# Performance work log

Hardware: AMD Instinct MI355X
Metric: run time of the kernel (lower is better)

The kernel has to match this reference:

```python
import jax, jax.numpy as jnp
import numpy as np

E, NH, NL, NP, DFFN = 256, 8, 4, 4, 1024
HD = E // NH
EPS = 1e-5
SHAPES = np.array([[128, 128], [64, 64], [32, 32], [16, 16]], np.int32)


def layer_norm(x, w, b):
    m = x.mean(-1, keepdims=True)
    v = ((x - m) ** 2).mean(-1, keepdims=True)
    return (x - m) * jax.lax.rsqrt(v + EPS) * w + b


def mha(q, k, v, in_w, in_b, out_w, out_b):
    # q: [Lq, B, E], k/v: [Lk, B, E]  (torch nn.MultiheadAttention, seq-first)
    Lq, B, _ = q.shape
    wq, wk, wv = jnp.split(in_w, 3, axis=0)
    bq, bk, bv = jnp.split(in_b, 3)
    qh = (q @ wq.T + bq).reshape(Lq, B, NH, HD)
    kh = (k @ wk.T + bk).reshape(k.shape[0], B, NH, HD)
    vh = (v @ wv.T + bv).reshape(v.shape[0], B, NH, HD)
    scores = jnp.einsum('qbhd,kbhd->bhqk', qh, kh) / jnp.sqrt(jnp.asarray(HD, q.dtype))
    attn = jax.nn.softmax(scores, axis=-1)
    out = jnp.einsum('bhqk,kbhd->qbhd', attn, vh).reshape(Lq, B, E)
    return out @ out_w.T + out_b


def deform_core(value, spatial_shapes, loc, w):
    # value: [bs, Lv, NH, HD]; loc: [bs, nq, NH, NL, NP, 2] in [0,1]; w: [bs, nq, NH, NL, NP]
    bs, _, nh, hd = value.shape
    nq = loc.shape[1]
    out = jnp.zeros((bs, nq, nh, hd), value.dtype)
    start = 0
    for l in range(len(spatial_shapes)):
        H, W = int(spatial_shapes[l][0]), int(spatial_shapes[l][1])
        val = value[:, start:start + H * W]  # [bs, H*W, nh, hd]
        start += H * W
        # grid_sample align_corners=False convention: pixel = loc*size - 0.5
        x = loc[:, :, :, l, :, 0] * W - 0.5  # [bs, nq, nh, NP]
        y = loc[:, :, :, l, :, 1] * H - 0.5
        x0 = jnp.floor(x); y0 = jnp.floor(y)
        lx = x - x0; ly = y - y0
        x0i = x0.astype(jnp.int32); y0i = y0.astype(jnp.int32)

        def gather(yi, xi):
            valid = ((xi >= 0) & (xi < W) & (yi >= 0) & (yi < H)).astype(value.dtype)
            idx = jnp.clip(yi, 0, H - 1) * W + jnp.clip(xi, 0, W - 1)  # [bs, nq, nh, NP]
            idx2 = idx.transpose(0, 1, 3, 2).reshape(bs, nq * NP, nh)
            g = jnp.take_along_axis(val, idx2[..., None], axis=1)  # [bs, nq*NP, nh, hd]
            g = g.reshape(bs, nq, NP, nh, hd).transpose(0, 1, 3, 2, 4)  # [bs, nq, nh, NP, hd]
            return g * valid[..., None]

        samp = (gather(y0i, x0i) * ((1 - lx) * (1 - ly))[..., None]
                + gather(y0i, x0i + 1) * (lx * (1 - ly))[..., None]
                + gather(y0i + 1, x0i) * ((1 - lx) * ly)[..., None]
                + gather(y0i + 1, x0i + 1) * (lx * ly)[..., None])
        out = out + (samp * w[:, :, :, l, :, None]).sum(axis=3)
    return out.reshape(bs, nq, nh * hd)


def fwd(tgt, tgt_pos, ref_pts, memory_support, memory,
        sa_in_w, sa_in_b, sa_out_w, sa_out_b,
        cs_in_w, cs_in_b, cs_out_w, cs_out_b,
        so_w, so_b, aw_w, aw_b, vp_w, vp_b, op_w, op_b,
        norm1_w, norm1_b, norm2_w, norm2_b, csn_w, csn_b, norm3_w, norm3_b,
        lin1_w, lin1_b, lin2_w, lin2_b, spatial_shapes):
    # --- self attention ---
    q = tgt + tgt_pos
    tgt = layer_norm(tgt + mha(q, q, tgt, sa_in_w, sa_in_b, sa_out_w, sa_out_b), norm2_w, norm2_b)
    # --- cross attention on support tokens ---
    ms = memory_support.transpose(1, 0, 2)  # [Ls, bs, E]
    tgt = layer_norm(tgt + mha(tgt + tgt_pos, ms, ms, cs_in_w, cs_in_b, cs_out_w, cs_out_b), csn_w, csn_b)
    # --- multi-scale deformable cross attention ---
    query = (tgt + tgt_pos).transpose(1, 0, 2)  # [bs, nq, E]
    ref = ref_pts.transpose(1, 0, 2, 3)  # [bs, nq, NL, 4]
    bs, nq = query.shape[:2]
    val = (memory.transpose(1, 0, 2) @ vp_w.T + vp_b).reshape(bs, -1, NH, HD)
    off = (query @ so_w.T + so_b).reshape(bs, nq, NH, NL, NP, 2)
    aw = jax.nn.softmax((query @ aw_w.T + aw_b).reshape(bs, nq, NH, NL * NP), axis=-1)
    aw = aw.reshape(bs, nq, NH, NL, NP)
    loc = ref[:, :, None, :, None, :2] + off / NP * ref[:, :, None, :, None, 2:] * 0.5
    out = deform_core(val, spatial_shapes, loc, aw) @ op_w.T + op_b  # [bs, nq, E]
    tgt = layer_norm(tgt + out.transpose(1, 0, 2), norm1_w, norm1_b)
    # --- FFN ---
    h = jax.nn.relu(tgt @ lin1_w.T + lin1_b)
    return layer_norm(tgt + (h @ lin2_w.T + lin2_b), norm3_w, norm3_b)


def setup_inputs():
    nq, bs, Ls = 900, 8, 100
    Lv = int((SHAPES[:, 0] * SHAPES[:, 1]).sum())
    keys = iter(jax.random.split(jax.random.key(0), 64))
    f = lambda *s: jax.random.normal(next(keys), s, jnp.float32)
    w = lambda o, i: f(o, i) * 0.02
    # sampling-offset bias mirrors torch _reset_parameters grid init
    thetas = np.arange(NH, dtype=np.float32) * (2.0 * np.pi / NH)
    grid = np.stack([np.cos(thetas), np.sin(thetas)], -1)
    grid = grid / np.abs(grid).max(-1, keepdims=True)
    grid = np.tile(grid.reshape(NH, 1, 1, 2), (1, NL, NP, 1)) * np.arange(1, NP + 1, dtype=np.float32).reshape(1, 1, NP, 1)
    xy = jax.random.uniform(next(keys), (nq, bs, NL, 2))
    wh = jax.random.uniform(next(keys), (nq, bs, NL, 2)) * 0.2 + 0.02
    return dict(
        tgt=f(nq, bs, E) * 0.1,
        tgt_pos=f(nq, bs, E) * 0.1,
        tgt_reference_points=jnp.concatenate([xy, wh], -1),
        memory_support=f(bs, Ls, E) * 0.1,
        memory=f(Lv, bs, E) * 0.1,
        memory_spatial_shapes=SHAPES,
        sa_in_w=w(3 * E, E), sa_in_b=jnp.zeros(3 * E), sa_out_w=w(E, E), sa_out_b=jnp.zeros(E),
        cs_in_w=w(3 * E, E), cs_in_b=jnp.zeros(3 * E), cs_out_w=w(E, E), cs_out_b=jnp.zeros(E),
        so_w=f(NH * NL * NP * 2, E) * 0.01, so_b=jnp.asarray(grid.reshape(-1)),
        aw_w=f(NH * NL * NP, E) * 0.01, aw_b=jnp.zeros(NH * NL * NP),
        vp_w=w(E, E), vp_b=jnp.zeros(E), op_w=w(E, E), op_b=jnp.zeros(E),
        norm1_w=jnp.ones(E), norm1_b=jnp.zeros(E),
        norm2_w=jnp.ones(E), norm2_b=jnp.zeros(E),
        csn_w=jnp.ones(E), csn_b=jnp.zeros(E),
        norm3_w=jnp.ones(E), norm3_b=jnp.zeros(E),
        lin1_w=w(DFFN, E), lin1_b=jnp.zeros(DFFN),
        lin2_w=w(E, DFFN), lin2_b=jnp.zeros(E),
    )


def reference(tgt, tgt_pos, tgt_reference_points, memory_support, memory, memory_spatial_shapes,
              sa_in_w, sa_in_b, sa_out_w, sa_out_b, cs_in_w, cs_in_b, cs_out_w, cs_out_b,
              so_w, so_b, aw_w, aw_b, vp_w, vp_b, op_w, op_b,
              norm1_w, norm1_b, norm2_w, norm2_b, csn_w, csn_b, norm3_w, norm3_b,
              lin1_w, lin1_b, lin2_w, lin2_b):
    return fwd(tgt, tgt_pos, tgt_reference_points, memory_support, memory,
               sa_in_w, sa_in_b, sa_out_w, sa_out_b,
               cs_in_w, cs_in_b, cs_out_w, cs_out_b,
               so_w, so_b, aw_w, aw_b, vp_w, vp_b, op_w, op_b,
               norm1_w, norm1_b, norm2_w, norm2_b, csn_w, csn_b, norm3_w, norm3_b,
               lin1_w, lin1_b, lin2_w, lin2_b, SHAPES)
```

## Files before the change

### kernel.cpp

```cpp
#include <hip/hip_runtime.h>
#include <hip/hip_bf16.h>


typedef __hip_bfloat16 bf16;
typedef __attribute__((ext_vector_type(8))) short short8;
typedef __attribute__((ext_vector_type(4))) float f32x4;

__device__ __forceinline__ float toF(bf16 x) { return __bfloat162float(x); }

__device__ __forceinline__ float ldF(const void* p, size_t i, int f32mode) {
    if (f32mode) return ((const float*)p)[i];
    return __bfloat162float(((const bf16*)p)[i]);
}
__device__ __forceinline__ void stF(void* p, size_t i, int f32mode, float v) {
    if (f32mode) ((float*)p)[i] = v;
    else ((bf16*)p)[i] = __float2bfloat16(v);
}
__device__ __forceinline__ int decode(int code, int fl) { return code == 2 ? fl : code; }

__device__ __forceinline__ short f2b(float x) {
    bf16 h = __float2bfloat16(x);
    return *(short*)&h;
}

__device__ __forceinline__ short8 loadFrag8(const void* p, size_t idx, int f32m) {
    short8 r;
    if (f32m) {
        const float4* q = (const float4*)((const float*)p + idx);
        float4 u = q[0];
        float4 v = q[1];
        r[0] = f2b(u.x); r[1] = f2b(u.y); r[2] = f2b(u.z); r[3] = f2b(u.w);
        r[4] = f2b(v.x); r[5] = f2b(v.y); r[6] = f2b(v.z); r[7] = f2b(v.w);
    } else {
        r = *(const short8*)((const bf16*)p + idx);
    }
    return r;
}

__global__ __launch_bounds__(256) void detect_kernel(
    const unsigned short* __restrict__ t, int* __restrict__ flag)
{
    __shared__ int bad;
    if (threadIdx.x == 0) bad = 0;
    __syncthreads();
    int my = 0;
    for (int k = 0; k < 8; k++) {
        unsigned u = t[threadIdx.x + 256 * k];
        unsigned e = (u >> 7) & 0xFF;
        if (e >= 0xC0) my = 1;
    }
    if (my) atomicOr(&bad, 1);
    __syncthreads();
    if (threadIdx.x == 0) *flag = bad;
}

__global__ __launch_bounds__(256) void dbg_kernel(bf16* out, int n, float v)
{
    int i = blockIdx.x * 256 + threadIdx.x;
    if (i < n) out[i] = __float2bfloat16(v);
}

template <bool RELU>
__global__ __launch_bounds__(256) void mgemm_kernel(
    const void* __restrict__ A, int lda, size_t aOff, int aCode,
    const void* __restrict__ W, size_t wOff,
    const void* __restrict__ bias, size_t bOff,
    bf16* __restrict__ C, int ldc,
    int M, int N, int K, const int* __restrict__ flagp)
{
    const int fl = *flagp;
    const int am = decode(aCode, fl);
    const int tid = threadIdx.x;
    const int lane = tid & 63;
    const int wv = tid >> 6;
    const int l15 = lane & 15;
    const int quad = lane >> 4;
    const int bm = blockIdx.y * 64 + wv * 16;
    const int bn = blockIdx.x * 64;

    const int ar = min(bm + l15, M - 1);
    const size_t aBase = aOff + (size_t)ar * lda + quad * 8;

    f32x4 acc[4] = {};

    for (int k0 = 0; k0 < K; k0 += 32) {
        short8 af = loadFrag8(A, aBase + k0, am);
#pragma unroll
        for (int nt = 0; nt < 4; nt++) {
            int n = bn + nt * 16 + l15;
            short8 bfr = loadFrag8(W, wOff + (size_t)n * K + quad * 8 + k0, fl);
            acc[nt] = __builtin_amdgcn_mfma_f32_16x16x32_bf16(af, bfr, acc[nt], 0, 0, 0);
        }
    }

#pragma unroll
    for (int nt = 0; nt < 4; nt++) {
        int n = bn + nt * 16 + l15;
        float bv = ldF(bias, bOff + n, fl);
#pragma unroll
        for (int r = 0; r < 4; r++) {
            int row = bm + quad * 4 + r;
            if (row < M) {
                float v = acc[nt][r] + bv;
                if (RELU) v = fmaxf(v, 0.f);
                C[(size_t)row * ldc + n] = __float2bfloat16(v);
            }
        }
    }
}

template <bool RELU>
__global__ __launch_bounds__(512) void mgemm_lds_kernel(
    const void* __restrict__ A, int lda, size_t aOff, int aCode,
    const void* __restrict__ W, size_t wOff,
    const void* __restrict__ bias, size_t bOff,
    bf16* __restrict__ C, int ldc,
    int M, int K, const int* __restrict__ flagp)
{
    const int fl = *flagp;
    const int am = decode(aCode, fl);
    const int tid = threadIdx.x;
    const int lane = tid & 63;
    const int w = tid >> 6;
    const int l15 = lane & 15;
    const int quad = lane >> 4;
    const int wr = w >> 2;
    const int wc = w & 3;
    const int bm = blockIdx.y * 128;
    const int bn = blockIdx.x * 256;

    __shared__ short Al[128][40];
    __shared__ short Bl[256][40];

    const int sRow = tid >> 2;
    const int sCb  = (tid & 3) * 8;
    const int gArow = min(bm + sRow, M - 1);
    const size_t aRowBase = aOff + (size_t)gArow * lda + sCb;
    const size_t wRowBase0 = wOff + (size_t)(bn + sRow) * K + sCb;
    const size_t wRowBase1 = wOff + (size_t)(bn + 128 + sRow) * K + sCb;

    f32x4 acc[4][4] = {};

    for (int k0 = 0; k0 < K; k0 += 32) {
        __syncthreads();
        *(short8*)&Al[sRow][sCb]       = loadFrag8(A, aRowBase + k0, am);
        *(short8*)&Bl[sRow][sCb]       = loadFrag8(W, wRowBase0 + k0, fl);
        *(short8*)&Bl[128 + sRow][sCb] = loadFrag8(W, wRowBase1 + k0, fl);
        __syncthreads();

        short8 a0 = *(const short8*)&Al[wr * 64 +  0 + l15][quad * 8];
        short8 a1 = *(const short8*)&Al[wr * 64 + 16 + l15][quad * 8];
        short8 a2 = *(const short8*)&Al[wr * 64 + 32 + l15][quad * 8];
        short8 a3 = *(const short8*)&Al[wr * 64 + 48 + l15][quad * 8];
#pragma unroll
        for (int nt = 0; nt < 4; nt++) {
            short8 b = *(const short8*)&Bl[wc * 64 + nt * 16 + l15][quad * 8];
            acc[0][nt] = __builtin_amdgcn_mfma_f32_16x16x32_bf16(a0, b, acc[0][nt], 0, 0, 0);
            acc[1][nt] = __builtin_amdgcn_mfma_f32_16x16x32_bf16(a1, b, acc[1][nt], 0, 0, 0);
            acc[2][nt] = __builtin_amdgcn_mfma_f32_16x16x32_bf16(a2, b, acc[2][nt], 0, 0, 0);
            acc[3][nt] = __builtin_amdgcn_mfma_f32_16x16x32_bf16(a3, b, acc[3][nt], 0, 0, 0);
        }
    }

#pragma unroll
    for (int nt = 0; nt < 4; nt++) {
        int n = bn + wc * 64 + nt * 16 + l15;
        float bv = ldF(bias, bOff + n, fl);
#pragma unroll
        for (int mt = 0; mt < 4; mt++) {
#pragma unroll
            for (int r = 0; r < 4; r++) {
                int row = bm + wr * 64 + mt * 16 + quad * 4 + r;
                if (row < M) {
                    float v = acc[mt][nt][r] + bv;
                    if (RELU) v = fmaxf(v, 0.f);
                    C[(size_t)row * ldc + n] = __float2bfloat16(v);
                }
            }
        }
    }
}

__global__ __launch_bounds__(256) void add_kernel(
    const void* __restrict__ A, int aCode, const void* __restrict__ B,
    bf16* __restrict__ out, int n, const int* __restrict__ flagp)
{
    const int fl = *flagp;
    const int am = decode(aCode, fl);
    int i = blockIdx.x * 256 + threadIdx.x;
    if (i < n) out[i] = __float2bfloat16(ldF(A, i, am) + ldF(B, i, fl));
}

__global__ __launch_bounds__(256) void ln_res_kernel(
    const bf16* __restrict__ A, const void* __restrict__ R, int rCode,
    const void* __restrict__ w, const void* __restrict__ b,
    void* __restrict__ out, int oCode, const int* __restrict__ flagp)
{
    const int fl = *flagp;
    const int rm = decode(rCode, fl);
    const int om = decode(oCode, fl);
    const int r = blockIdx.x, tid = threadIdx.x;
    const size_t o = (size_t)r * 256 + tid;
    float x = toF(A[o]) + ldF(R, o, rm);
    __shared__ float red[256];
    red[tid] = x;
    __syncthreads();
    for (int st = 128; st > 0; st >>= 1) {
        if (tid < st) red[tid] += red[tid + st];
        __syncthreads();
    }
    float mean = red[0] * (1.f / 256.f);
    __syncthreads();
    float dx = x - mean;
    red[tid] = dx * dx;
    __syncthreads();
    for (int st = 128; st > 0; st >>= 1) {
        if (tid < st) red[tid] += red[tid + st];
        __syncthreads();
    }
    float var = red[0] * (1.f / 256.f);
    float y = dx * rsqrtf(var + 1e-5f) * ldF(w, tid, fl) + ldF(b, tid, fl);
    stF(out, o, om, y);
}

__global__ __launch_bounds__(256) void transpose_v_kernel(
    const bf16* __restrict__ V, int vs0, int vs1,
    bf16* __restrict__ VT, int Lk, int lkp)
{
    int i = blockIdx.x * 256 + threadIdx.x;
    int kp = i % lkp;
    int ch = i / lkp;
    int b = ch >> 8, hd = ch & 255;
    bf16 v = __float2bfloat16(0.f);
    if (kp < Lk) v = V[(size_t)kp * vs0 + (size_t)b * vs1 + hd];
    VT[i] = v;
}

__global__ __launch_bounds__(256) void fattn_kernel(
    const bf16* __restrict__ Q, int qs0, int qs1,
    const bf16* __restrict__ K, int ks0, int ks1,
    const bf16* __restrict__ VT, int lkp,
    bf16* __restrict__ O, int Lk, float scale)
{
    const int bh = blockIdx.x;
    const int b = bh >> 3, h = bh & 7;
    const int qt = blockIdx.y;
    const int tid = threadIdx.x;
    const int w = tid >> 6;
    const int lane = tid & 63;
    const int l15 = lane & 15;
    const int quad = lane >> 4;

    __shared__ short Pl[4][16][72];

    const int q0 = qt * 64 + w * 16;
    const int qr = min(q0 + l15, 899);
    short8 aq = *(const short8*)(Q + (size_t)qr * qs0 + (size_t)b * qs1 + h * 32 + quad * 8);

    f32x4 accO0 = {}, accO1 = {};
    float mrow[4] = {-1e30f, -1e30f, -1e30f, -1e30f};
    float lrow[4] = {0.f, 0.f, 0.f, 0.f};

    const bf16* Kb = K + (size_t)b * ks1 + h * 32 + quad * 8;
    const bf16* VTb = VT + (size_t)(b * 256 + h * 32) * lkp;

    const int nkt = (Lk + 63) >> 6;
    for (int kt = 0; kt < nkt; kt++) {
        const int k0 = kt * 64;
        float sv[4][4];
#pragma unroll
        for (int nt = 0; nt < 4; nt++) {
            int kk = k0 + nt * 16 + l15;
            int krow = min(kk, Lk - 1);
            short8 bk = *(const short8*)(Kb + (size_t)krow * ks0);
            f32x4 z = {};
            f32x4 s = __builtin_amdgcn_mfma_f32_16x16x32_bf16(aq, bk, z, 0, 0, 0);
            bool ok = kk < Lk;
#pragma unroll
            for (int r = 0; r < 4; r++) sv[nt][r] = ok ? s[r] * scale : -1e30f;
        }
        float mnew[4], fr[4];
#pragma unroll
        for (int r = 0; r < 4; r++) {
            float t = fmaxf(fmaxf(sv[0][r], sv[1][r]), fmaxf(sv[2][r], sv[3][r]));
            t = fmaxf(t, __shfl_xor(t, 1));
            t = fmaxf(t, __shfl_xor(t, 2));
            t = fmaxf(t, __shfl_xor(t, 4));
            t = fmaxf(t, __shfl_xor(t, 8));
            mnew[r] = fmaxf(mrow[r], t);
            fr[r] = __expf(mrow[r] - mnew[r]);
            mrow[r] = mnew[r];
        }
#pragma unroll
        for (int r = 0; r < 4; r++) {
            float p0 = __expf(sv[0][r] - mnew[r]);
            float p1 = __expf(sv[1][r] - mnew[r]);
            float p2 = __expf(sv[2][r] - mnew[r]);
            float p3 = __expf(sv[3][r] - mnew[r]);
            int row = quad * 4 + r;
            Pl[w][row][l15]      = f2b(p0);
            Pl[w][row][16 + l15] = f2b(p1);
            Pl[w][row][32 + l15] = f2b(p2);
            Pl[w][row][48 + l15] = f2b(p3);
            float t = p0 + p1 + p2 + p3;
            t += __shfl_xor(t, 1);
            t += __shfl_xor(t, 2);
            t += __shfl_xor(t, 4);
            t += __shfl_xor(t, 8);
            lrow[r] = lrow[r] * fr[r] + t;
            accO0[r] *= fr[r];
            accO1[r] *= fr[r];
        }
#pragma unroll
        for (int kt2 = 0; kt2 < 2; kt2++) {
            short8 pa = *(const short8*)&Pl[w][l15][kt2 * 32 + quad * 8];
            short8 v0 = *(const short8*)(VTb + (size_t)l15 * lkp + k0 + kt2 * 32 + quad * 8);
            short8 v1 = *(const short8*)(VTb + (size_t)(16 + l15) * lkp + k0 + kt2 * 32 + quad * 8);
            accO0 = __builtin_amdgcn_mfma_f32_16x16x32_bf16(pa, v0, accO0, 0, 0, 0);
            accO1 = __builtin_amdgcn_mfma_f32_16x16x32_bf16(pa, v1, accO1, 0, 0, 0);
        }
    }
#pragma unroll
    for (int r = 0; r < 4; r++) {
        int q = q0 + quad * 4 + r;
        if (q < 900) {
            float inv = 1.f / lrow[r];
            size_t o = ((size_t)q * 8 + b) * 256 + h * 32;
            O[o + l15]      = __float2bfloat16(accO0[r] * inv);
            O[o + 16 + l15] = __float2bfloat16(accO1[r] * inv);
        }
    }
}

__device__ __forceinline__ float sample_one(const bf16* __restrict__ valb,
                                            int base, int HW, int yi, int xi,
                                            int hd32)
{
    bool valid = (xi >= 0) && (xi < HW) && (yi >= 0) && (yi < HW);
    int ix = min(max(xi, 0), HW - 1);
    int iy = min(max(yi, 0), HW - 1);
    size_t idx = (size_t)(base + iy * HW + ix) * 2048 + hd32;
    float v = toF(valb[idx]);
    return valid ? v : 0.f;
}

__global__ __launch_bounds__(256) void deform_kernel(
    const bf16* __restrict__ val,
    const bf16* __restrict__ off,
    const bf16* __restrict__ awl,
    const void* __restrict__ refp,
    bf16* __restrict__ samp, const int* __restrict__ flagp)
{
    const int fl = *flagp;
    const int levH[4] = {128, 64, 32, 16};
    const int levS[4] = {0, 16384, 20480, 21504};
    const int r = blockIdx.x;
    const int tid = threadIdx.x;
    const int h = tid >> 5, d = tid & 31;
    const int hd32 = h * 32 + d;

    const bf16* valb = val + (size_t)(r & 7) * 256;

    const bf16* lg = awl + (size_t)r * 128 + h * 16;
    float w[16];
    float mx = -1e30f;
#pragma unroll
    for (int i = 0; i < 16; i++) { w[i] = toF(lg[i]); mx = fmaxf(mx, w[i]); }
    float sm = 0.f;
#pragma unroll
    for (int i = 0; i < 16; i++) { w[i] = expf(w[i] - mx); sm += w[i]; }
    float inv = 1.f / sm;

    const bf16* offr = off + (size_t)r * 256 + h * 32;
    float acc = 0.f;
#pragma unroll
    for (int l = 0; l < 4; l++) {
        const int HW = levH[l];
        const int base = levS[l];
        float rx = ldF(refp, (size_t)r * 16 + l * 4 + 0, fl);
        float ry = ldF(refp, (size_t)r * 16 + l * 4 + 1, fl);
        float rw = ldF(refp, (size_t)r * 16 + l * 4 + 2, fl);
        float rh = ldF(refp, (size_t)r * 16 + l * 4 + 3, fl);
#pragma unroll
        for (int p = 0; p < 4; p++) {
            float ox = toF(offr[l * 8 + p * 2 + 0]);
            float oy = toF(offr[l * 8 + p * 2 + 1]);
            float locx = rx + ox * 0.125f * rw;
            float locy = ry + oy * 0.125f * rh;
            float x = locx * HW - 0.5f;
            float y = locy * HW - 0.5f;
            float x0f = floorf(x), y0f = floorf(y);
            int x0 = (int)x0f, y0 = (int)y0f;
            float fx = x - x0f, fy = y - y0f;
            float wgt = w[l * 4 + p] * inv;
            float s00 = sample_one(valb, base, HW, y0,     x0,     hd32);
            float s01 = sample_one(valb, base, HW, y0,     x0 + 1, hd32);
            float s10 = sample_one(valb, base, HW, y0 + 1, x0,     hd32);
            float s11 = sample_one(valb, base, HW, y0 + 1, x0 + 1, hd32);
            acc += wgt * (s00 * (1.f - fx) * (1.f - fy) + s01 * fx * (1.f - fy) +
                          s10 * (1.f - fx) * fy + s11 * fx * fy);
        }
    }
    samp[(size_t)r * 256 + tid] = __float2bfloat16(acc);
}

extern "C" void kernel_launch(void* const* d_in, const int* in_sizes, int n_in,
                              void* d_out, int out_size, void* d_ws, size_t ws_size,
                              hipStream_t stream)
{
    (void)in_sizes; (void)n_in;
    const void* tgt      = d_in[0];
    const void* tgt_pos  = d_in[1];
    const void* refp     = d_in[2];
    const void* mem_sup  = d_in[3];
    const void* memory   = d_in[4];
    const void* sa_in_w  = d_in[6];
    const void* sa_in_b  = d_in[7];
    const void* sa_out_w = d_in[8];
    const void* sa_out_b = d_in[9];
    const void* cs_in_w  = d_in[10];
    const void* cs_in_b  = d_in[11];
    const void* cs_out_w = d_in[12];
    const void* cs_out_b = d_in[13];
    const void* so_w = d_in[14];
    const void* so_b = d_in[15];
    const void* aw_w = d_in[16];
    const void* aw_b = d_in[17];
    const void* vp_w = d_in[18];
    const void* vp_b = d_in[19];
    const void* op_w = d_in[20];
    const void* op_b = d_in[21];
    const void* n1w = d_in[22];
    const void* n1b = d_in[23];
    const void* n2w = d_in[24];
    const void* n2b = d_in[25];
    const void* csnw = d_in[26];
    const void* csnb = d_in[27];
    const void* n3w = d_in[28];
    const void* n3b = d_in[29];
    const void* l1w = d_in[30];
    const void* l1b = d_in[31];
    const void* l2w = d_in[32];
    const void* l2b = d_in[33];

    const int S = 900 * 8 * 256;
    const size_t NEEDED = 133496836;
    const dim3 blk(256);
    const dim3 blk2(512);

    if (ws_size < NEEDED) {
        dbg_kernel<<<(out_size + 255) / 256, blk, 0, stream>>>(
            (bf16*)d_out, out_size, (float)(ws_size >> 20));
        return;
    }

    char* base = (char*)d_ws;
    float* T5 = (float*)base;
    bf16* B1  = (bf16*)(base + 7372800);
    bf16* B2  = (bf16*)(base + 11059200);
    bf16* B3  = (bf16*)(base + 18432000);
    bf16* B4  = (bf16*)(base + 22249472);
    bf16* B5  = (bf16*)(base + 25935872);
    bf16* VAL = (bf16*)(base + 29622272);
    bf16* H   = (bf16*)(base + 118751232);
    int* FL   = (int*)(base + 133496832);

    const float scale = 0.1767766953f;
    const int MT = 7200;
    const int gy = 57;

    detect_kernel<<<1, blk, 0, stream>>>((const unsigned short*)tgt, FL);

    add_kernel<<<MT, blk, 0, stream>>>(tgt, 2, tgt_pos, B1, S, FL);
    mgemm_lds_kernel<false><<<dim3(2, gy), blk2, 0, stream>>>(
        B1, 256, 0, 0, sa_in_w, 0, sa_in_b, 0, B2, 512, MT, 256, FL);
    mgemm_lds_kernel<false><<<dim3(1, gy), blk2, 0, stream>>>(
        tgt, 256, 0, 2, sa_in_w, 131072, sa_in_b, 512, B3, 256, MT, 256, FL);
    transpose_v_kernel<<<7680, blk, 0, stream>>>(B3, 2048, 256, (bf16*)T5, 900, 960);
    fattn_kernel<<<dim3(64, 15), blk, 0, stream>>>(
        B2, 4096, 512, B2 + 256, 4096, 512, (bf16*)T5, 960, B4, 900, scale);
    mgemm_lds_kernel<false><<<dim3(1, gy), blk2, 0, stream>>>(
        B4, 256, 0, 0, sa_out_w, 0, sa_out_b, 0, B5, 256, MT, 256, FL);
    ln_res_kernel<<<MT, blk, 0, stream>>>(B5, tgt, 2, n2w, n2b, T5, 1, FL);

    add_kernel<<<MT, blk, 0, stream>>>(T5, 1, tgt_pos, B1, S, FL);
    mgemm_lds_kernel<false><<<dim3(1, gy), blk2, 0, stream>>>(
        B1, 256, 0, 0, cs_in_w, 0, cs_in_b, 0, B2, 256, MT, 256, FL);
    mgemm_lds_kernel<false><<<dim3(2, 7), blk2, 0, stream>>>(
        mem_sup, 256, 0, 2, cs_in_w, 65536, cs_in_b, 256, B3, 512, 800, 256, FL);
    transpose_v_kernel<<<1024, blk, 0, stream>>>(B3 + 256, 512, 51200, B1, 100, 128);
    fattn_kernel<<<dim3(64, 15), blk, 0, stream>>>(
        B2, 2048, 256, B3, 512, 51200, B1, 128, B4, 100, scale);
    mgemm_lds_kernel<false><<<dim3(1, gy), blk2, 0, stream>>>(
        B4, 256, 0, 0, cs_out_w, 0, cs_out_b, 0, B5, 256, MT, 256, FL);
    ln_res_kernel<<<MT, blk, 0, stream>>>(B5, T5, 1, csnw, csnb, T5, 1, FL);

    add_kernel<<<MT, blk, 0, stream>>>(T5, 1, tgt_pos, B1, S, FL);
    mgemm_lds_kernel<false><<<dim3(1, gy), blk2, 0, stream>>>(
        B1, 256, 0, 0, so_w, 0, so_b, 0, B4, 256, MT, 256, FL);
    mgemm_kernel<false><<<dim3(2, 113), blk, 0, stream>>>(
        B1, 256, 0, 0, aw_w, 0, aw_b, 0, B5, 128, MT, 128, 256, FL);
    mgemm_lds_kernel<false><<<dim3(1, 1360), blk2, 0, stream>>>(
        memory, 256, 0, 2, vp_w, 0, vp_b, 0, VAL, 256, 174080, 256, FL);
    deform_kernel<<<7200, blk, 0, stream>>>(VAL, B4, B5, refp, B1, FL);
    mgemm_lds_kernel<false><<<dim3(1, gy), blk2, 0, stream>>>(
        B1, 256, 0, 0, op_w, 0, op_b, 0, B5, 256, MT, 256, FL);
    ln_res_kernel<<<MT, blk, 0, stream>>>(B5, T5, 1, n1w, n1b, T5, 1, FL);

    mgemm_lds_kernel<true><<<dim3(4, gy), blk2, 0, stream>>>(
        T5, 256, 0, 1, l1w, 0, l1b, 0, H, 1024, MT, 256, FL);
    mgemm_lds_kernel<false><<<dim3(1, gy), blk2, 0, stream>>>(
        H, 1024, 0, 0, l2w, 0, l2b, 0, B5, 256, MT, 1024, FL);
    ln_res_kernel<<<MT, blk, 0, stream>>>(B5, T5, 1, n3w, n3b, d_out, 2, FL);
}
```

Before: 927.9 us.

## Fuse positional add into GEMM A-load and use smaller 64x128 GEMM tiles

Adds a 64x128-tile LDS GEMM kernel whose A-tile load can optionally add a residual tensor (tgt + pos) on the fly. This removes the separate add kernels and their intermediate buffer round-trips. All the 7200-row GEMMs move to this kernel, which gives more blocks and better occupancy on the GPU for small M. The large value-projection GEMM keeps the old 128x256 tile. The old per-wave mgemm_kernel is removed. The risk is lower reuse per block, and the fused A-load is scalar per element when the residual is present.

Result: faster. 842.7 us (-9.2%).

```diff
diff --git a/kernel.cpp b/kernel.cpp
--- a/kernel.cpp
+++ b/kernel.cpp
@@ -37,6 +37,15 @@
     return r;
 }
 
+__device__ __forceinline__ short8 loadFragF(const void* A, size_t ia, int am,
+                                            const void* R, int rm) {
+    if (R == nullptr) return loadFrag8(A, ia, am);
+    short8 o;
+#pragma unroll
+    for (int j = 0; j < 8; j++) o[j] = f2b(ldF(A, ia + j, am) + ldF(R, ia + j, rm));
+    return o;
+}
+
 __global__ __launch_bounds__(256) void detect_kernel(
     const unsigned short* __restrict__ t, int* __restrict__ flag)
 {
@@ -58,55 +67,6 @@
 {
     int i = blockIdx.x * 256 + threadIdx.x;
     if (i < n) out[i] = __float2bfloat16(v);
-}
-
-template <bool RELU>
-__global__ __launch_bounds__(256) void mgemm_kernel(
-    const void* __restrict__ A, int lda, size_t aOff, int aCode,
-    const void* __restrict__ W, size_t wOff,
-    const void* __restrict__ bias, size_t bOff,
-    bf16* __restrict__ C, int ldc,
-    int M, int N, int K, const int* __restrict__ flagp)
-{
-    const int fl = *flagp;
-    const int am = decode(aCode, fl);
-    const int tid = threadIdx.x;
-    const int lane = tid & 63;
-    const int wv = tid >> 6;
-    const int l15 = lane & 15;
-    const int quad = lane >> 4;
-    const int bm = blockIdx.y * 64 + wv * 16;
-    const int bn = blockIdx.x * 64;
-
-    const int ar = min(bm + l15, M - 1);
-    const size_t aBase = aOff + (size_t)ar * lda + quad * 8;
-
-    f32x4 acc[4] = {};
-
-    for (int k0 = 0; k0 < K; k0 += 32) {
-        short8 af = loadFrag8(A, aBase + k0, am);
-#pragma unroll
-        for (int nt = 0; nt < 4; nt++) {
-            int n = bn + nt * 16 + l15;
-            short8 bfr = loadFrag8(W, wOff + (size_t)n * K + quad * 8 + k0, fl);
-            acc[nt] = __builtin_amdgcn_mfma_f32_16x16x32_bf16(af, bfr, acc[nt], 0, 0, 0);
-        }
-    }
-
-#pragma unroll
-    for (int nt = 0; nt < 4; nt++) {
-        int n = bn + nt * 16 + l15;
-        float bv = ldF(bias, bOff + n, fl);
-#pragma unroll
-        for (int r = 0; r < 4; r++) {
-            int row = bm + quad * 4 + r;
-            if (row < M) {
-                float v = acc[nt][r] + bv;
-                if (RELU) v = fmaxf(v, 0.f);
-                C[(size_t)row * ldc + n] = __float2bfloat16(v);
-            }
-        }
-    }
 }
 
 template <bool RELU>
@@ -163,16 +123,15 @@
     }
 
 #pragma unroll
-    for (int nt = 0; nt < 4; nt++) {
-        int n = bn + wc * 64 + nt * 16 + l15;
-        float bv = ldF(bias, bOff + n, fl);
-#pragma unroll
-        for (int mt = 0; mt < 4; mt++) {
-#pragma unroll
-            for (int r = 0; r < 4; r++) {
-                int row = bm + wr * 64 + mt * 16 + quad * 4 + r;
-                if (row < M) {
-                    float v = acc[mt][nt][r] + bv;
+    for (int mt = 0; mt < 4; mt++) {
+#pragma unroll
+        for (int r = 0; r < 4; r++) {
+            int row = bm + wr * 64 + mt * 16 + quad * 4 + r;
+            if (row < M) {
+#pragma unroll
+                for (int nt = 0; nt < 4; nt++) {
+                    int n = bn + wc * 64 + nt * 16 + l15;
+                    float v = acc[mt][nt][r] + ldF(bias, bOff + n, fl);
                     if (RELU) v = fmaxf(v, 0.f);
                     C[(size_t)row * ldc + n] = __float2bfloat16(v);
                 }
@@ -181,14 +140,68 @@
     }
 }
 
-__global__ __launch_bounds__(256) void add_kernel(
-    const void* __restrict__ A, int aCode, const void* __restrict__ B,
-    bf16* __restrict__ out, int n, const int* __restrict__ flagp)
+template <bool RELU>
+__global__ __launch_bounds__(512) void mgemm_lds64_kernel(
+    const void* __restrict__ A, int lda, size_t aOff, int aCode,
+    const void* __restrict__ R, int rCode,
+    const void* __restrict__ W, size_t wOff,
+    const void* __restrict__ bias, size_t bOff,
+    bf16* __restrict__ C, int ldc,
+    int M, int K, const int* __restrict__ flagp)
 {
     const int fl = *flagp;
     const int am = decode(aCode, fl);
-    int i = blockIdx.x * 256 + threadIdx.x;
-    if (i < n) out[i] = __float2bfloat16(ldF(A, i, am) + ldF(B, i, fl));
+    const int rm = decode(rCode, fl);
+    const int tid = threadIdx.x;
+    const int lane = tid & 63;
+    const int w = tid >> 6;
+    const int l15 = lane & 15;
+    const int quad = lane >> 4;
+    const int wr = w >> 1;
+    const int wc = w & 1;
+    const int bm = blockIdx.y * 64;
+    const int bn = blockIdx.x * 128;
+
+    __shared__ short Al[64][40];
+    __shared__ short Bl[128][40];
+
+    const int sRow = tid >> 2;
+    const int sCb  = (tid & 3) * 8;
+    const int gArow = min(bm + (sRow & 63), M - 1);
+    const size_t aRowBase = aOff + (size_t)gArow * lda + sCb;
+    const size_t wRowBase = wOff + (size_t)(bn + sRow) * K + sCb;
+
+    f32x4 acc[4] = {};
+
+    for (int k0 = 0; k0 < K; k0 += 32) {
+        __syncthreads();
+        if (tid < 256) {
+            *(short8*)&Al[sRow][sCb] = loadFragF(A, aRowBase + k0, am, R, rm);
+        }
+        *(short8*)&Bl[sRow][sCb] = loadFrag8(W, wRowBase + k0, fl);
+        __syncthreads();
+
+        short8 a = *(const short8*)&Al[wr * 16 + l15][quad * 8];
+#pragma unroll
+        for (int nt = 0; nt < 4; nt++) {
+            short8 b = *(const short8*)&Bl[wc * 64 + nt * 16 + l15][quad * 8];
+            acc[nt] = __builtin_amdgcn_mfma_f32_16x16x32_bf16(a, b, acc[nt], 0, 0, 0);
+        }
+    }
+
+#pragma unroll
+    for (int r = 0; r < 4; r++) {
+        int row = bm + wr * 16 + quad * 4 + r;
+        if (row < M) {
+#pragma unroll
+            for (int nt = 0; nt < 4; nt++) {
+                int n = bn + wc * 64 + nt * 16 + l15;
+                float v = acc[nt][r] + ldF(bias, bOff + n, fl);
+                if (RELU) v = fmaxf(v, 0.f);
+                C[(size_t)row * ldc + n] = __float2bfloat16(v);
+            }
+        }
+    }
 }
 
 __global__ __launch_bounds__(256) void ln_res_kernel(
@@ -467,49 +480,55 @@
 
     const float scale = 0.1767766953f;
     const int MT = 7200;
-    const int gy = 57;
+    const int gy = 113;
 
     detect_kernel<<<1, blk, 0, stream>>>((const unsigned short*)tgt, FL);
 
-    add_kernel<<<MT, blk, 0, stream>>>(tgt, 2, tgt_pos, B1, S, FL);
-    mgemm_lds_kernel<false><<<dim3(2, gy), blk2, 0, stream>>>(
-        B1, 256, 0, 0, sa_in_w, 0, sa_in_b, 0, B2, 512, MT, 256, FL);
-    mgemm_lds_kernel<false><<<dim3(1, gy), blk2, 0, stream>>>(
-        tgt, 256, 0, 2, sa_in_w, 131072, sa_in_b, 512, B3, 256, MT, 256, FL);
+    mgemm_lds64_kernel<false><<<dim3(4, gy), blk2, 0, stream>>>(
+        tgt, 256, 0, 2, tgt_pos, 2, sa_in_w, 0, sa_in_b, 0,
+        B2, 512, MT, 256, FL);
+    mgemm_lds64_kernel<false><<<dim3(2, gy), blk2, 0, stream>>>(
+        tgt, 256, 0, 2, nullptr, 0, sa_in_w, 131072, sa_in_b, 512,
+        B3, 256, MT, 256, FL);
     transpose_v_kernel<<<7680, blk, 0, stream>>>(B3, 2048, 256, (bf16*)T5, 900, 960);
     fattn_kernel<<<dim3(64, 15), blk, 0, stream>>>(
         B2, 4096, 512, B2 + 256, 4096, 512, (bf16*)T5, 960, B4, 900, scale);
-    mgemm_lds_kernel<false><<<dim3(1, gy), blk2, 0, stream>>>(
-        B4, 256, 0, 0, sa_out_w, 0, sa_out_b, 0, B5, 256, MT, 256, FL);
+    mgemm_lds64_kernel<false><<<dim3(2, gy), blk2, 0, stream>>>(
+        B4, 256, 0, 0, nullptr, 0, sa_out_w, 0, sa_out_b, 0,
+        B5, 256, MT, 256, FL);
     ln_res_kernel<<<MT, blk, 0, stream>>>(B5, tgt, 2, n2w, n2b, T5, 1, FL);
 
-    add_kernel<<<MT, blk, 0, stream>>>(T5, 1, tgt_pos, B1, S, FL);
-    mgemm_lds_kernel<false><<<dim3(1, gy), blk2, 0, stream>>>(
-        B1, 256, 0, 0, cs_in_w, 0, cs_in_b, 0, B2, 256, MT, 256, FL);
-    mgemm_lds_kernel<false><<<dim3(2, 7), blk2, 0, stream>>>(
-        mem_sup, 256, 0, 2, cs_in_w, 65536, cs_in_b, 256, B3, 512, 800, 256, FL);
+    mgemm_lds64_kernel<false><<<dim3(2, gy), blk2, 0, stream>>>(
+        T5, 256, 0, 1, tgt_pos, 2, cs_in_w, 0, cs_in_b, 0,
+        B2, 256, MT, 256, FL);
+    mgemm_lds64_kernel<false><<<dim3(4, 13), blk2, 0, stream>>>(
+        mem_sup, 256, 0, 2, nullptr, 0, cs_in_w, 65536, cs_in_b, 256,
+        B3, 512, 800, 256, FL);
     transpose_v_kernel<<<1024, blk, 0, stream>>>(B3 + 256, 512, 51200, B1, 100, 128);
     fattn_kernel<<<dim3(64, 15), blk, 0, stream>>>(
         B2, 2048, 256, B3, 512, 51200, B1, 128, B4, 100, scale);
-    mgemm_lds_kernel<false><<<dim3(1, gy), blk2, 0, stream>>>(
-        B4, 256, 0, 0, cs_out_w, 0, cs_out_b, 0, B5, 256, MT, 256, FL);
+    mgemm_lds64_kernel<false><<<dim3(2, gy), blk2, 0, stream>>>(
+        B4, 256, 0, 0, nullptr, 0, cs_out_w, 0, cs_out_b, 0,
+        B5, 256, MT, 256, FL);
     ln_res_kernel<<<MT, blk, 0, stream>>>(B5, T5, 1, csnw, csnb, T5, 1, FL);
 
-    add_kernel<<<MT, blk, 0, stream>>>(T5, 1, tgt_pos, B1, S, FL);
-    mgemm_lds_kernel<false><<<dim3(1, gy), blk2, 0, stream>>>(
-        B1, 256, 0, 0, so_w, 0, so_b, 0, B4, 256, MT, 256, FL);
-    mgemm_kernel<false><<<dim3(2, 113), blk, 0, stream>>>(
-        B1, 256, 0, 0, aw_w, 0, aw_b, 0, B5, 128, MT, 128, 256, FL);
+    mgemm_lds64_kernel<false><<<dim3(2, gy), blk2, 0, stream>>>(
+        T5, 256, 0, 1, tgt_pos, 2, so_w, 0, so_b, 0,
+        B4, 256, MT, 256, FL);
+    mgemm_lds64_kernel<false><<<dim3(1, gy), blk2, 0, stream>>>(
+        T5, 256, 0, 1, tgt_pos, 2, aw_w, 0, aw_b, 0,
+        B5, 128, MT, 256, FL);
     mgemm_lds_kernel<false><<<dim3(1, 1360), blk2, 0, stream>>>(
         memory, 256, 0, 2, vp_w, 0, vp_b, 0, VAL, 256, 174080, 256, FL);
     deform_kernel<<<7200, blk, 0, stream>>>(VAL, B4, B5, refp, B1, FL);
-    mgemm_lds_kernel<false><<<dim3(1, gy), blk2, 0, stream>>>(
-        B1, 256, 0, 0, op_w, 0, op_b, 0, B5, 256, MT, 256, FL);
+    mgemm_lds64_kernel<false><<<dim3(2, gy), blk2, 0, stream>>>(
+        B1, 256, 0, 0, nullptr, 0, op_w, 0, op_b, 0,
+        B5, 256, MT, 256, FL);
     ln_res_kernel<<<MT, blk, 0, stream>>>(B5, T5, 1, n1w, n1b, T5, 1, FL);
 
-    mgemm_lds_kernel<true><<<dim3(4, gy), blk2, 0, stream>>>(
-        T5, 256, 0, 1, l1w, 0, l1b, 0, H, 1024, MT, 256, FL);
-    mgemm_lds_kernel<false><<<dim3(1, gy), blk2, 0, stream>>>(
-        H, 1024, 0, 0, l2w, 0, l2b, 0, B5, 256, MT, 1024, FL);
+    mgemm_lds64_kernel<true><<<dim3(8, gy), blk2, 0, stream>>>(
+        T5, 256, 0, 1, nullptr, 0, l1w, 0, l1b, 0, H, 1024, MT, 256, FL);
+    mgemm_lds64_kernel<false><<<dim3(2, gy), blk2, 0, stream>>>(
+        H, 1024, 0, 0, nullptr, 0, l2w, 0, l2b, 0, B5, 256, MT, 1024, FL);
     ln_res_kernel<<<MT, blk, 0, stream>>>(B5, T5, 1, n3w, n3b, d_out, 2, FL);
 }
```
